# Kernel optimization log

Measured on AMD Instinct MI355X. Metric: run time of the kernel, lower is better.

The kernel has to match this reference:

```python
import jax, jax.numpy as jnp
import numpy as np

NUM_HEADS = 16
D_K = 8  # == n_qubits


def setup_inputs() -> dict:
    key = jax.random.key(0)
    k1, k2, k3 = jax.random.split(key, 3)
    x = jax.random.normal(k1, (4, 2048, 128), dtype=jnp.float32)
    # trainable RX angles, one per qubit (tq.RX has_params=True)
    theta = jax.random.normal(k2, (D_K,), dtype=jnp.float32)
    # out_proj: Linear(embed_dim, embed_dim, bias=False)
    w_out = jax.random.normal(k3, (128, 128), dtype=jnp.float32) * (1.0 / np.sqrt(128.0))
    return {"x": x, "theta": theta, "w_out": w_out}


def quantum_features(x, theta):
    # x: [b, s, e]. Per head of size d_k: encode RX(x_i), trainable RX(theta_i)
    # (composes to RX(x_i + theta_i)), CNOT ladder [i, i+1], measure PauliZ.
    # Heisenberg picture: Z_w -> Z_0...Z_w, so <Z_w> = prod_{i<=w} cos(x_i + theta_i).
    b, s, e = x.shape
    heads = x.reshape(b, s, NUM_HEADS, D_K)
    return jnp.cumprod(jnp.cos(heads + theta), axis=-1)  # [b, s, h, d_k]


def reference(x, theta, w_out):
    b, s, e = x.shape
    # q == k == v: same shared q_layer applied to the same x three times.
    qkv = quantum_features(x, theta)            # [b, s, h, d_k]
    q = qkv.transpose(0, 2, 1, 3)               # [b, h, s, d_k]
    scores = jnp.einsum('bhqd,bhkd->bhqk', q, q) / np.sqrt(D_K)
    attn = jax.nn.softmax(scores, axis=-1)      # dropout is identity at eval
    out = jnp.einsum('bhqk,bhkd->bhqd', attn, q)
    out = out.transpose(0, 2, 1, 3).reshape(b, s, e)
    return out @ w_out.T
```

## Files before the change

### kernel.cpp

```cpp
#include <hip/hip_runtime.h>

#define BATCH 4
#define SEQ   2048
#define EMB   128
#define NH    16
#define DK    8

#define QSCALE 0.510069726f

typedef _Float16 v2h __attribute__((ext_vector_type(2)));
typedef _Float16 v4h __attribute__((ext_vector_type(4)));
typedef float    v4f __attribute__((ext_vector_type(4)));

#define CHUNK 1024
#define VTP   1032

__launch_bounds__(512, 4)
__global__ void attn_kernel(const float* __restrict__ x,
                            const float* __restrict__ theta,
                            _Float16* __restrict__ Ah ) {
  __shared__ __align__(16) _Float16 Kl[CHUNK * 8];
  __shared__ __align__(16) _Float16 VT[16][VTP];

  const int tid  = threadIdx.x;
  const int L    = tid & 63;
  const int wv   = tid >> 6;
  const int quad = L >> 4;
  const int ln   = L & 15;
  const int bh     = blockIdx.x >> 3;
  const int qchunk = blockIdx.x & 7;
  const int qb     = qchunk * 256 + wv * 32;
  const int b = bh >> 4;
  const int h = bh & 15;

  float th[DK];
#pragma unroll
  for (int i = 0; i < DK; ++i) th[i] = theta[i];

  for (int i = tid; i < 8 * VTP / 4; i += 512) {
    v4h v = (i < VTP / 4) ? (v4h){(_Float16)1.f, (_Float16)1.f,
                                  (_Float16)1.f, (_Float16)1.f}
                          : (v4h){0, 0, 0, 0};
    *(v4h*)(&VT[8][0] + i * 4) = v;
  }

  const int c0 = qchunk >> 2;
  v4h qf[2];
  v4f acc[2];
  acc[0] = (v4f){0.f, 0.f, 0.f, 0.f};
  acc[1] = (v4f){0.f, 0.f, 0.f, 0.f};
  const v4f zf = (v4f){0.f, 0.f, 0.f, 0.f};

  for (int cc = 0; cc < 2; ++cc) {
    const int c = cc ? (1 - c0) : c0;
    if (cc) __syncthreads();

    {
      const int k2 = tid * 2;
      const float* xp = x + ((size_t)b * SEQ + c * CHUNK + k2) * EMB + h * DK;
      const float4 a0 = *(const float4*)(xp);
      const float4 a1 = *(const float4*)(xp + 4);
      const float4 b0 = *(const float4*)(xp + EMB);
      const float4 b1 = *(const float4*)(xp + EMB + 4);

      float r0[8], r1[8];
      r0[0] = __cosf(a0.x + th[0]);
      r0[1] = r0[0] * __cosf(a0.y + th[1]);
      r0[2] = r0[1] * __cosf(a0.z + th[2]);
      r0[3] = r0[2] * __cosf(a0.w + th[3]);
      r0[4] = r0[3] * __cosf(a1.x + th[4]);
      r0[5] = r0[4] * __cosf(a1.y + th[5]);
      r0[6] = r0[5] * __cosf(a1.z + th[6]);
      r0[7] = r0[6] * __cosf(a1.w + th[7]);
      r1[0] = __cosf(b0.x + th[0]);
      r1[1] = r1[0] * __cosf(b0.y + th[1]);
      r1[2] = r1[1] * __cosf(b0.z + th[2]);
      r1[3] = r1[2] * __cosf(b0.w + th[3]);
      r1[4] = r1[3] * __cosf(b1.x + th[4]);
      r1[5] = r1[4] * __cosf(b1.y + th[5]);
      r1[6] = r1[5] * __cosf(b1.z + th[6]);
      r1[7] = r1[6] * __cosf(b1.w + th[7]);

      _Float16 h0[8], h1[8];
#pragma unroll
      for (int i = 0; i < 8; ++i) { h0[i] = (_Float16)r0[i]; h1[i] = (_Float16)r1[i]; }

      union { v4h v[2]; float4 f; } u0, u1;
      u0.v[0] = (v4h){h0[0], h0[1], h0[2], h0[3]};
      u0.v[1] = (v4h){h0[4], h0[5], h0[6], h0[7]};
      u1.v[0] = (v4h){h1[0], h1[1], h1[2], h1[3]};
      u1.v[1] = (v4h){h1[4], h1[5], h1[6], h1[7]};
      *(float4*)&Kl[k2 * 8]     = u0.f;
      *(float4*)&Kl[k2 * 8 + 8] = u1.f;

#pragma unroll
      for (int d = 0; d < 8; ++d) {
        v2h w = {h0[d], h1[d]};
        *(v2h*)&VT[d][k2] = w;
      }
    }
    __syncthreads();

    if (cc == 0) {
      const v4h qsc = {(_Float16)QSCALE, (_Float16)QSCALE,
                       (_Float16)QSCALE, (_Float16)QSCALE};
#pragma unroll
      for (int t = 0; t < 2; ++t) {
        const int lrow = qb - c0 * CHUNK + t * 16 + ln;
        v4h q = {0, 0, 0, 0};
        if (quad < 2) q = *(const v4h*)&Kl[lrow * 8 + quad * 4];
        qf[t] = q * qsc;
      }
    }

    for (int t16 = 0; t16 < CHUNK / 16; ++t16) {
      const v4h kv = *(const v4h*)&Kl[(t16 * 16 + ln) * 8 + (quad & 1) * 4];
      const v4h kf = (quad < 2) ? kv : (v4h){0, 0, 0, 0};
      const v4h vt = *(const v4h*)&VT[ln][t16 * 16 + quad * 4];
#pragma unroll
      for (int t = 0; t < 2; ++t) {
        const v4f s = __builtin_amdgcn_mfma_f32_16x16x16f16(kf, qf[t], zf, 0, 0, 0);
        v4h pb;
        pb[0] = (_Float16)__builtin_amdgcn_exp2f(s[0]);
        pb[1] = (_Float16)__builtin_amdgcn_exp2f(s[1]);
        pb[2] = (_Float16)__builtin_amdgcn_exp2f(s[2]);
        pb[3] = (_Float16)__builtin_amdgcn_exp2f(s[3]);
        acc[t] = __builtin_amdgcn_mfma_f32_16x16x16f16(vt, pb, acc[t], 0, 0, 0);
      }
    }
  }

#pragma unroll
  for (int t = 0; t < 2; ++t) {
    const float den = __shfl(acc[t][0], 32 + ln, 64);
    const float inv = 1.0f / den;
    if (quad < 2) {
      const int qrow = qb + t * 16 + ln;
      v4h o = {(_Float16)(acc[t][0] * inv), (_Float16)(acc[t][1] * inv),
               (_Float16)(acc[t][2] * inv), (_Float16)(acc[t][3] * inv)};
      *(v4h*)(Ah + ((size_t)b * SEQ + qrow) * EMB + h * DK + quad * 4) = o;
    }
  }
}

__launch_bounds__(256, 1)
__global__ void proj_kernel(const _Float16* __restrict__ Ah,
                            const float* __restrict__ W,
                            float* __restrict__ out) {
  __shared__ __align__(16) _Float16 Ahs[64][136];
  __shared__ __align__(16) _Float16 Whs[128][136];

  const int tid  = threadIdx.x;
  const int L    = tid & 63;
  const int wv   = tid >> 6;
  const int quad = L >> 4;
  const int ln   = L & 15;
  const int rowbase = blockIdx.x * 64;

#pragma unroll
  for (int it = 0; it < 4; ++it) {
    const int idx = it * 256 + tid;
    const int r  = idx >> 4;
    const int c8 = idx & 15;
    *(uint4*)&Ahs[r][c8 * 8] =
        *(const uint4*)(Ah + (size_t)(rowbase + r) * EMB + c8 * 8);
  }
#pragma unroll
  for (int it = 0; it < 16; ++it) {
    const int idx = it * 256 + tid;
    const int n  = idx >> 5;
    const int c4 = idx & 31;
    const float4 w = *(const float4*)(W + (size_t)n * EMB + c4 * 4);
    v4h wh = {(_Float16)w.x, (_Float16)w.y, (_Float16)w.z, (_Float16)w.w};
    *(v4h*)&Whs[n][c4 * 4] = wh;
  }
  __syncthreads();

  v4f acc[8];
#pragma unroll
  for (int nt = 0; nt < 8; ++nt) acc[nt] = (v4f){0.f, 0.f, 0.f, 0.f};

#pragma unroll
  for (int k8 = 0; k8 < 8; ++k8) {
    const v4h af = *(const v4h*)&Ahs[wv * 16 + ln][k8 * 16 + quad * 4];
#pragma unroll
    for (int nt = 0; nt < 8; ++nt) {
      const v4h bf = *(const v4h*)&Whs[nt * 16 + ln][k8 * 16 + quad * 4];
      acc[nt] = __builtin_amdgcn_mfma_f32_16x16x16f16(af, bf, acc[nt], 0, 0, 0);
    }
  }

#pragma unroll
  for (int nt = 0; nt < 8; ++nt) {
    const int col = nt * 16 + ln;
#pragma unroll
    for (int r = 0; r < 4; ++r) {
      out[(size_t)(rowbase + wv * 16 + quad * 4 + r) * EMB + col] = acc[nt][r];
    }
  }
}

extern "C" void kernel_launch(void* const* d_in, const int* in_sizes, int n_in,
                              void* d_out, int out_size, void* d_ws, size_t ws_size,
                              hipStream_t stream) {
  const float* x     = (const float*)d_in[0];
  const float* theta = (const float*)d_in[1];
  const float* w_out = (const float*)d_in[2];
  float* out = (float*)d_out;

  _Float16* Ah = (_Float16*)d_ws;

  attn_kernel<<<dim3(512), dim3(512), 0, stream>>>(x, theta, Ah);

  proj_kernel<<<dim3((BATCH * SEQ) / 64), dim3(256), 0, stream>>>(Ah, w_out, out);
}
```

Before: 97.89 us.

## Halve attention work per wave and block, split projection over columns

The attention kernel now gives each wave one 16-query tile instead of two and streams keys in 512-key chunks, launching twice as many blocks with a higher occupancy hint. Softmax exponentials are packed to fp16 with a single pack-with-round-toward-zero conversion instead of separate conversions. The projection kernel is split into two 64-column halves across a second grid dimension to expose more blocks. The aim is more parallelism and better latency hiding. In exchange, each block recomputes the quantum features for all keys, doubling that recompute in total, and each K/V LDS load now feeds one tile instead of two.

```diff
diff --git a/kernel.cpp b/kernel.cpp
--- a/kernel.cpp
+++ b/kernel.cpp
@@ -10,12 +10,14 @@
 
 typedef _Float16 v2h __attribute__((ext_vector_type(2)));
 typedef _Float16 v4h __attribute__((ext_vector_type(4)));
+typedef __fp16   v2fp __attribute__((ext_vector_type(2)));
 typedef float    v4f __attribute__((ext_vector_type(4)));
 
-#define CHUNK 1024
-#define VTP   1032
+#define CHUNK  512
+#define NCHUNK (SEQ / CHUNK)
+#define VTP    520
 
-__launch_bounds__(512, 4)
+__launch_bounds__(512, 8)
 __global__ void attn_kernel(const float* __restrict__ x,
                             const float* __restrict__ theta,
                             _Float16* __restrict__ Ah ) {
@@ -24,12 +26,12 @@
 
   const int tid  = threadIdx.x;
   const int L    = tid & 63;
-  const int wv   = tid >> 6;
   const int quad = L >> 4;
   const int ln   = L & 15;
-  const int bh     = blockIdx.x >> 3;
-  const int qchunk = blockIdx.x & 7;
-  const int qb     = qchunk * 256 + wv * 32;
+  const int wv   = tid >> 6;
+  const int bh     = blockIdx.x >> 4;
+  const int qchunk = blockIdx.x & 15;
+  const int qb     = qchunk * 128 + wv * 16;
   const int b = bh >> 4;
   const int h = bh & 15;
 
@@ -45,110 +47,82 @@
   }
 
   const int c0 = qchunk >> 2;
-  v4h qf[2];
-  v4f acc[2];
-  acc[0] = (v4f){0.f, 0.f, 0.f, 0.f};
-  acc[1] = (v4f){0.f, 0.f, 0.f, 0.f};
+  v4h qf = {0, 0, 0, 0};
+  v4f acc = (v4f){0.f, 0.f, 0.f, 0.f};
   const v4f zf = (v4f){0.f, 0.f, 0.f, 0.f};
 
-  for (int cc = 0; cc < 2; ++cc) {
-    const int c = cc ? (1 - c0) : c0;
+  for (int cc = 0; cc < NCHUNK; ++cc) {
+    const int c = (c0 + cc) & (NCHUNK - 1);
     if (cc) __syncthreads();
 
     {
-      const int k2 = tid * 2;
-      const float* xp = x + ((size_t)b * SEQ + c * CHUNK + k2) * EMB + h * DK;
+      const float* xp = x + ((size_t)b * SEQ + c * CHUNK + tid) * EMB + h * DK;
       const float4 a0 = *(const float4*)(xp);
       const float4 a1 = *(const float4*)(xp + 4);
-      const float4 b0 = *(const float4*)(xp + EMB);
-      const float4 b1 = *(const float4*)(xp + EMB + 4);
 
-      float r0[8], r1[8];
-      r0[0] = __cosf(a0.x + th[0]);
-      r0[1] = r0[0] * __cosf(a0.y + th[1]);
-      r0[2] = r0[1] * __cosf(a0.z + th[2]);
-      r0[3] = r0[2] * __cosf(a0.w + th[3]);
-      r0[4] = r0[3] * __cosf(a1.x + th[4]);
-      r0[5] = r0[4] * __cosf(a1.y + th[5]);
-      r0[6] = r0[5] * __cosf(a1.z + th[6]);
-      r0[7] = r0[6] * __cosf(a1.w + th[7]);
-      r1[0] = __cosf(b0.x + th[0]);
-      r1[1] = r1[0] * __cosf(b0.y + th[1]);
-      r1[2] = r1[1] * __cosf(b0.z + th[2]);
-      r1[3] = r1[2] * __cosf(b0.w + th[3]);
-      r1[4] = r1[3] * __cosf(b1.x + th[4]);
-      r1[5] = r1[4] * __cosf(b1.y + th[5]);
-      r1[6] = r1[5] * __cosf(b1.z + th[6]);
-      r1[7] = r1[6] * __cosf(b1.w + th[7]);
+      float r[8];
+      r[0] = __cosf(a0.x + th[0]);
+      r[1] = r[0] * __cosf(a0.y + th[1]);
+      r[2] = r[1] * __cosf(a0.z + th[2]);
+      r[3] = r[2] * __cosf(a0.w + th[3]);
+      r[4] = r[3] * __cosf(a1.x + th[4]);
+      r[5] = r[4] * __cosf(a1.y + th[5]);
+      r[6] = r[5] * __cosf(a1.z + th[6]);
+      r[7] = r[6] * __cosf(a1.w + th[7]);
 
-      _Float16 h0[8], h1[8];
+      _Float16 hv[8];
 #pragma unroll
-      for (int i = 0; i < 8; ++i) { h0[i] = (_Float16)r0[i]; h1[i] = (_Float16)r1[i]; }
+      for (int i = 0; i < 8; ++i) hv[i] = (_Float16)r[i];
 
-      union { v4h v[2]; float4 f; } u0, u1;
-      u0.v[0] = (v4h){h0[0], h0[1], h0[2], h0[3]};
-      u0.v[1] = (v4h){h0[4], h0[5], h0[6], h0[7]};
-      u1.v[0] = (v4h){h1[0], h1[1], h1[2], h1[3]};
-      u1.v[1] = (v4h){h1[4], h1[5], h1[6], h1[7]};
-      *(float4*)&Kl[k2 * 8]     = u0.f;
-      *(float4*)&Kl[k2 * 8 + 8] = u1.f;
+      union { v4h v[2]; float4 f; } u;
+      u.v[0] = (v4h){hv[0], hv[1], hv[2], hv[3]};
+      u.v[1] = (v4h){hv[4], hv[5], hv[6], hv[7]};
+      *(float4*)&Kl[tid * 8] = u.f;
 
 #pragma unroll
-      for (int d = 0; d < 8; ++d) {
-        v2h w = {h0[d], h1[d]};
-        *(v2h*)&VT[d][k2] = w;
-      }
+      for (int d = 0; d < 8; ++d) VT[d][tid] = hv[d];
     }
     __syncthreads();
 
     if (cc == 0) {
       const v4h qsc = {(_Float16)QSCALE, (_Float16)QSCALE,
                        (_Float16)QSCALE, (_Float16)QSCALE};
-#pragma unroll
-      for (int t = 0; t < 2; ++t) {
-        const int lrow = qb - c0 * CHUNK + t * 16 + ln;
-        v4h q = {0, 0, 0, 0};
-        if (quad < 2) q = *(const v4h*)&Kl[lrow * 8 + quad * 4];
-        qf[t] = q * qsc;
-      }
+      const int lrow = qb - c0 * CHUNK + ln;
+      if (quad < 2) qf = *(const v4h*)&Kl[lrow * 8 + quad * 4] * qsc;
     }
 
     for (int t16 = 0; t16 < CHUNK / 16; ++t16) {
       const v4h kv = *(const v4h*)&Kl[(t16 * 16 + ln) * 8 + (quad & 1) * 4];
       const v4h kf = (quad < 2) ? kv : (v4h){0, 0, 0, 0};
       const v4h vt = *(const v4h*)&VT[ln][t16 * 16 + quad * 4];
-#pragma unroll
-      for (int t = 0; t < 2; ++t) {
-        const v4f s = __builtin_amdgcn_mfma_f32_16x16x16f16(kf, qf[t], zf, 0, 0, 0);
-        v4h pb;
-        pb[0] = (_Float16)__builtin_amdgcn_exp2f(s[0]);
-        pb[1] = (_Float16)__builtin_amdgcn_exp2f(s[1]);
-        pb[2] = (_Float16)__builtin_amdgcn_exp2f(s[2]);
-        pb[3] = (_Float16)__builtin_amdgcn_exp2f(s[3]);
-        acc[t] = __builtin_amdgcn_mfma_f32_16x16x16f16(vt, pb, acc[t], 0, 0, 0);
-      }
+      const v4f s = __builtin_amdgcn_mfma_f32_16x16x16f16(kf, qf, zf, 0, 0, 0);
+      union { v2fp p[2]; v4h v; } pk;
+      pk.p[0] = __builtin_amdgcn_cvt_pkrtz(__builtin_amdgcn_exp2f(s[0]),
+                                           __builtin_amdgcn_exp2f(s[1]));
+      pk.p[1] = __builtin_amdgcn_cvt_pkrtz(__builtin_amdgcn_exp2f(s[2]),
+                                           __builtin_amdgcn_exp2f(s[3]));
+      acc = __builtin_amdgcn_mfma_f32_16x16x16f16(vt, pk.v, acc, 0, 0, 0);
     }
   }
 
-#pragma unroll
-  for (int t = 0; t < 2; ++t) {
-    const float den = __shfl(acc[t][0], 32 + ln, 64);
+  {
+    const float den = __shfl(acc[0], 32 + ln, 64);
     const float inv = 1.0f / den;
     if (quad < 2) {
-      const int qrow = qb + t * 16 + ln;
-      v4h o = {(_Float16)(acc[t][0] * inv), (_Float16)(acc[t][1] * inv),
-               (_Float16)(acc[t][2] * inv), (_Float16)(acc[t][3] * inv)};
+      const int qrow = qb + ln;
+      v4h o = {(_Float16)(acc[0] * inv), (_Float16)(acc[1] * inv),
+               (_Float16)(acc[2] * inv), (_Float16)(acc[3] * inv)};
       *(v4h*)(Ah + ((size_t)b * SEQ + qrow) * EMB + h * DK + quad * 4) = o;
     }
   }
 }
 
-__launch_bounds__(256, 1)
+__launch_bounds__(256, 4)
 __global__ void proj_kernel(const _Float16* __restrict__ Ah,
                             const float* __restrict__ W,
                             float* __restrict__ out) {
   __shared__ __align__(16) _Float16 Ahs[64][136];
-  __shared__ __align__(16) _Float16 Whs[128][136];
+  __shared__ __align__(16) _Float16 Whs[64][136];
 
   const int tid  = threadIdx.x;
   const int L    = tid & 63;
@@ -156,6 +130,7 @@
   const int quad = L >> 4;
   const int ln   = L & 15;
   const int rowbase = blockIdx.x * 64;
+  const int colbase = blockIdx.y * 64;
 
 #pragma unroll
   for (int it = 0; it < 4; ++it) {
@@ -166,33 +141,33 @@
         *(const uint4*)(Ah + (size_t)(rowbase + r) * EMB + c8 * 8);
   }
 #pragma unroll
-  for (int it = 0; it < 16; ++it) {
+  for (int it = 0; it < 8; ++it) {
     const int idx = it * 256 + tid;
     const int n  = idx >> 5;
     const int c4 = idx & 31;
-    const float4 w = *(const float4*)(W + (size_t)n * EMB + c4 * 4);
+    const float4 w = *(const float4*)(W + (size_t)(colbase + n) * EMB + c4 * 4);
     v4h wh = {(_Float16)w.x, (_Float16)w.y, (_Float16)w.z, (_Float16)w.w};
     *(v4h*)&Whs[n][c4 * 4] = wh;
   }
   __syncthreads();
 
-  v4f acc[8];
+  v4f acc[4];
 #pragma unroll
-  for (int nt = 0; nt < 8; ++nt) acc[nt] = (v4f){0.f, 0.f, 0.f, 0.f};
+  for (int nt = 0; nt < 4; ++nt) acc[nt] = (v4f){0.f, 0.f, 0.f, 0.f};
 
 #pragma unroll
   for (int k8 = 0; k8 < 8; ++k8) {
     const v4h af = *(const v4h*)&Ahs[wv * 16 + ln][k8 * 16 + quad * 4];
 #pragma unroll
-    for (int nt = 0; nt < 8; ++nt) {
+    for (int nt = 0; nt < 4; ++nt) {
       const v4h bf = *(const v4h*)&Whs[nt * 16 + ln][k8 * 16 + quad * 4];
       acc[nt] = __builtin_amdgcn_mfma_f32_16x16x16f16(af, bf, acc[nt], 0, 0, 0);
     }
   }
 
 #pragma unroll
-  for (int nt = 0; nt < 8; ++nt) {
-    const int col = nt * 16 + ln;
+  for (int nt = 0; nt < 4; ++nt) {
+    const int col = colbase + nt * 16 + ln;
 #pragma unroll
     for (int r = 0; r < 4; ++r) {
       out[(size_t)(rowbase + wv * 16 + quad * 4 + r) * EMB + col] = acc[nt][r];
@@ -210,7 +185,7 @@
 
   _Float16* Ah = (_Float16*)d_ws;
 
-  attn_kernel<<<dim3(512), dim3(512), 0, stream>>>(x, theta, Ah);
+  attn_kernel<<<dim3(1024), dim3(512), 0, stream>>>(x, theta, Ah);
 
-  proj_kernel<<<dim3((BATCH * SEQ) / 64), dim3(256), 0, stream>>>(Ah, w_out, out);
+  proj_kernel<<<dim3((BATCH * SEQ) / 64, 2), dim3(256), 0, stream>>>(Ah, w_out, out);
 }
```

Result: faster. 95.92 us (-2.0%).

## Split attention into smaller blocks with more key chunks; split projection columns

Applied to the files above, without the earlier changes.

The attention kernel moves from 512-thread blocks over two 1024-key chunks to 256-thread blocks over four 512-key chunks. This doubles the grid and halves LDS per block, aiming at higher occupancy and better latency hiding. The softmax exp results are now packed with cvt_pkrtz, the inner key loop is unrolled by 4, and the redundant masking of the K fragment is dropped by zero-initialising the Q fragments. The projection kernel is split across two column halves to put more blocks in flight. In exchange, each key chunk's cosine features are now recomputed by twice as many blocks, and every block pays for more barriers.

```diff
diff --git a/kernel.cpp b/kernel.cpp
--- a/kernel.cpp
+++ b/kernel.cpp
@@ -10,12 +10,14 @@
 
 typedef _Float16 v2h __attribute__((ext_vector_type(2)));
 typedef _Float16 v4h __attribute__((ext_vector_type(4)));
+typedef __fp16   v2fp __attribute__((ext_vector_type(2)));
 typedef float    v4f __attribute__((ext_vector_type(4)));
 
-#define CHUNK 1024
-#define VTP   1032
-
-__launch_bounds__(512, 4)
+#define CHUNK  512
+#define NCHUNK (SEQ / CHUNK)
+#define VTP    520
+
+__launch_bounds__(256, 6)
 __global__ void attn_kernel(const float* __restrict__ x,
                             const float* __restrict__ theta,
                             _Float16* __restrict__ Ah ) {
@@ -24,12 +26,12 @@
 
   const int tid  = threadIdx.x;
   const int L    = tid & 63;
-  const int wv   = tid >> 6;
   const int quad = L >> 4;
   const int ln   = L & 15;
-  const int bh     = blockIdx.x >> 3;
-  const int qchunk = blockIdx.x & 7;
-  const int qb     = qchunk * 256 + wv * 32;
+  const int wv   = tid >> 6;
+  const int bh     = blockIdx.x >> 4;
+  const int qchunk = blockIdx.x & 15;
+  const int qb     = qchunk * 128 + wv * 32;
   const int b = bh >> 4;
   const int h = bh & 15;
 
@@ -37,7 +39,7 @@
 #pragma unroll
   for (int i = 0; i < DK; ++i) th[i] = theta[i];
 
-  for (int i = tid; i < 8 * VTP / 4; i += 512) {
+  for (int i = tid; i < 8 * VTP / 4; i += 256) {
     v4h v = (i < VTP / 4) ? (v4h){(_Float16)1.f, (_Float16)1.f,
                                   (_Float16)1.f, (_Float16)1.f}
                           : (v4h){0, 0, 0, 0};
@@ -45,14 +47,14 @@
   }
 
   const int c0 = qchunk >> 2;
-  v4h qf[2];
+  v4h qf[2] = {{0, 0, 0, 0}, {0, 0, 0, 0}};
   v4f acc[2];
   acc[0] = (v4f){0.f, 0.f, 0.f, 0.f};
   acc[1] = (v4f){0.f, 0.f, 0.f, 0.f};
   const v4f zf = (v4f){0.f, 0.f, 0.f, 0.f};
 
-  for (int cc = 0; cc < 2; ++cc) {
-    const int c = cc ? (1 - c0) : c0;
+  for (int cc = 0; cc < NCHUNK; ++cc) {
+    const int c = (c0 + cc) & (NCHUNK - 1);
     if (cc) __syncthreads();
 
     {
@@ -104,28 +106,26 @@
     if (cc == 0) {
       const v4h qsc = {(_Float16)QSCALE, (_Float16)QSCALE,
                        (_Float16)QSCALE, (_Float16)QSCALE};
-#pragma unroll
-      for (int t = 0; t < 2; ++t) {
-        const int lrow = qb - c0 * CHUNK + t * 16 + ln;
-        v4h q = {0, 0, 0, 0};
-        if (quad < 2) q = *(const v4h*)&Kl[lrow * 8 + quad * 4];
-        qf[t] = q * qsc;
+      const int lbase = qb - c0 * CHUNK + ln;
+      if (quad < 2) {
+        qf[0] = *(const v4h*)&Kl[(lbase)      * 8 + quad * 4] * qsc;
+        qf[1] = *(const v4h*)&Kl[(lbase + 16) * 8 + quad * 4] * qsc;
       }
     }
 
+#pragma unroll 4
     for (int t16 = 0; t16 < CHUNK / 16; ++t16) {
-      const v4h kv = *(const v4h*)&Kl[(t16 * 16 + ln) * 8 + (quad & 1) * 4];
-      const v4h kf = (quad < 2) ? kv : (v4h){0, 0, 0, 0};
+      const v4h kf = *(const v4h*)&Kl[(t16 * 16 + ln) * 8 + (quad & 1) * 4];
       const v4h vt = *(const v4h*)&VT[ln][t16 * 16 + quad * 4];
 #pragma unroll
       for (int t = 0; t < 2; ++t) {
         const v4f s = __builtin_amdgcn_mfma_f32_16x16x16f16(kf, qf[t], zf, 0, 0, 0);
-        v4h pb;
-        pb[0] = (_Float16)__builtin_amdgcn_exp2f(s[0]);
-        pb[1] = (_Float16)__builtin_amdgcn_exp2f(s[1]);
-        pb[2] = (_Float16)__builtin_amdgcn_exp2f(s[2]);
-        pb[3] = (_Float16)__builtin_amdgcn_exp2f(s[3]);
-        acc[t] = __builtin_amdgcn_mfma_f32_16x16x16f16(vt, pb, acc[t], 0, 0, 0);
+        union { v2fp p[2]; v4h v; } pk;
+        pk.p[0] = __builtin_amdgcn_cvt_pkrtz(__builtin_amdgcn_exp2f(s[0]),
+                                             __builtin_amdgcn_exp2f(s[1]));
+        pk.p[1] = __builtin_amdgcn_cvt_pkrtz(__builtin_amdgcn_exp2f(s[2]),
+                                             __builtin_amdgcn_exp2f(s[3]));
+        acc[t] = __builtin_amdgcn_mfma_f32_16x16x16f16(vt, pk.v, acc[t], 0, 0, 0);
       }
     }
   }
@@ -143,12 +143,12 @@
   }
 }
 
-__launch_bounds__(256, 1)
+__launch_bounds__(256, 4)
 __global__ void proj_kernel(const _Float16* __restrict__ Ah,
                             const float* __restrict__ W,
                             float* __restrict__ out) {
   __shared__ __align__(16) _Float16 Ahs[64][136];
-  __shared__ __align__(16) _Float16 Whs[128][136];
+  __shared__ __align__(16) _Float16 Whs[64][136];
 
   const int tid  = threadIdx.x;
   const int L    = tid & 63;
@@ -156,6 +156,7 @@
   const int quad = L >> 4;
   const int ln   = L & 15;
   const int rowbase = blockIdx.x * 64;
+  const int colbase = blockIdx.y * 64;
 
 #pragma unroll
   for (int it = 0; it < 4; ++it) {
@@ -166,33 +167,33 @@
         *(const uint4*)(Ah + (size_t)(rowbase + r) * EMB + c8 * 8);
   }
 #pragma unroll
-  for (int it = 0; it < 16; ++it) {
+  for (int it = 0; it < 8; ++it) {
     const int idx = it * 256 + tid;
     const int n  = idx >> 5;
     const int c4 = idx & 31;
-    const float4 w = *(const float4*)(W + (size_t)n * EMB + c4 * 4);
+    const float4 w = *(const float4*)(W + (size_t)(colbase + n) * EMB + c4 * 4);
     v4h wh = {(_Float16)w.x, (_Float16)w.y, (_Float16)w.z, (_Float16)w.w};
     *(v4h*)&Whs[n][c4 * 4] = wh;
   }
   __syncthreads();
 
-  v4f acc[8];
-#pragma unroll
-  for (int nt = 0; nt < 8; ++nt) acc[nt] = (v4f){0.f, 0.f, 0.f, 0.f};
+  v4f acc[4];
+#pragma unroll
+  for (int nt = 0; nt < 4; ++nt) acc[nt] = (v4f){0.f, 0.f, 0.f, 0.f};
 
 #pragma unroll
   for (int k8 = 0; k8 < 8; ++k8) {
     const v4h af = *(const v4h*)&Ahs[wv * 16 + ln][k8 * 16 + quad * 4];
 #pragma unroll
-    for (int nt = 0; nt < 8; ++nt) {
+    for (int nt = 0; nt < 4; ++nt) {
       const v4h bf = *(const v4h*)&Whs[nt * 16 + ln][k8 * 16 + quad * 4];
       acc[nt] = __builtin_amdgcn_mfma_f32_16x16x16f16(af, bf, acc[nt], 0, 0, 0);
     }
   }
 
 #pragma unroll
-  for (int nt = 0; nt < 8; ++nt) {
-    const int col = nt * 16 + ln;
+  for (int nt = 0; nt < 4; ++nt) {
+    const int col = colbase + nt * 16 + ln;
 #pragma unroll
     for (int r = 0; r < 4; ++r) {
       out[(size_t)(rowbase + wv * 16 + quad * 4 + r) * EMB + col] = acc[nt][r];
@@ -210,7 +211,7 @@
 
   _Float16* Ah = (_Float16*)d_ws;
 
-  attn_kernel<<<dim3(512), dim3(512), 0, stream>>>(x, theta, Ah);
-
-  proj_kernel<<<dim3((BATCH * SEQ) / 64), dim3(256), 0, stream>>>(Ah, w_out, out);
+  attn_kernel<<<dim3(1024), dim3(256), 0, stream>>>(x, theta, Ah);
+
+  proj_kernel<<<dim3((BATCH * SEQ) / 64, 2), dim3(256), 0, stream>>>(Ah, w_out, out);
 }
```

Result: faster. 94.16 us (-3.8%).
